# Kernel tuning notes

Measured on AMD Instinct MI355X. Metric: run time of the kernel, lower is better.

Reference implementation:

```python
import jax, jax.numpy as jnp
import numpy as np
from jax import lax

GAMMA = 2.0
BLANK = 0
NEG = -1e30  # log-space 'zero'
T, B, C, L = 1000, 64, 256, 100


def setup_inputs() -> dict:
    key = jax.random.key(0)
    k1, k2 = jax.random.split(key)
    # valid log-probabilities, as produced by a model's log_softmax head
    log_probs = jax.nn.log_softmax(jax.random.normal(k1, (T, B, C), dtype=jnp.float32), axis=-1)
    # concatenated targets, blank (0) excluded as CTC requires
    targets = jax.random.randint(k2, (B * L,), 1, C, dtype=jnp.int32)
    input_lengths = jnp.full((B,), T, dtype=jnp.int32)
    target_lengths = jnp.full((B,), L, dtype=jnp.int32)
    return {"log_probs": log_probs, "targets": targets,
            "input_lengths": input_lengths, "target_lengths": target_lengths}


def _ctc_loss(log_probs, targets2d, input_lengths, target_lengths):
    # log_probs: (T,B,C); targets2d: (B,L). Returns per-sample NLL (B,).
    Tt, Bb, _ = log_probs.shape
    Ll = targets2d.shape[1]
    S = 2 * Ll + 1  # extended label sequence: blank interleaved
    ext = jnp.full((Bb, S), BLANK, dtype=jnp.int32).at[:, 1::2].set(targets2d)
    # emission log-probs for each extended symbol: (T,B,S)
    emit = jnp.take_along_axis(log_probs, jnp.broadcast_to(ext[None], (Tt, Bb, S)), axis=2)
    # skip-transition allowed where symbol is non-blank and differs from s-2
    allow2 = jnp.concatenate(
        [jnp.zeros((Bb, 2), bool), (ext[:, 2:] != BLANK) & (ext[:, 2:] != ext[:, :-2])], axis=1)

    def shiftk(a, k):
        return jnp.pad(a, ((0, 0), (k, 0)), constant_values=NEG)[:, :S]

    alpha0 = jnp.full((Bb, S), NEG, jnp.float32).at[:, 0].set(emit[0, :, 0]).at[:, 1].set(emit[0, :, 1])

    def step(alpha, e):
        a1 = shiftk(alpha, 1)
        a2 = jnp.where(allow2, shiftk(alpha, 2), NEG)
        m = jnp.maximum(jnp.maximum(alpha, a1), a2)
        new = m + jnp.log(jnp.exp(alpha - m) + jnp.exp(a1 - m) + jnp.exp(a2 - m)) + e
        return new, new

    _, rest = lax.scan(step, alpha0, emit[1:])
    alphas = jnp.concatenate([alpha0[None], rest], axis=0)  # (T,B,S)
    b = jnp.arange(Bb)
    last = alphas[input_lengths - 1, b]  # (B,S) at each sample's final step
    ll = jnp.logaddexp(last[b, 2 * target_lengths], last[b, 2 * target_lengths - 1])
    # zero_infinity=True semantics
    return jnp.where(ll > NEG / 2, -ll, 0.0)


def reference(log_probs, targets, input_lengths, target_lengths):
    targets2d = targets.reshape(B, L)
    loss = _ctc_loss(log_probs, targets2d, input_lengths, target_lengths)  # (B,)
    # focal weights: mean-over-time prob of each target symbol (computed under no_grad in torch)
    mean_probs = jnp.exp(log_probs).mean(axis=0)  # (B,C)
    target_probs = lax.stop_gradient(
        jnp.take_along_axis(mean_probs, targets2d, axis=1).reshape(-1))  # (B*L,)
    focal_weight = (1.0 - target_probs) ** GAMMA
    # torch broadcasting quirk: (total,) * (B,1) -> (B,total); mean over all
    return (focal_weight[None, :] * loss[:, None]).mean()
```

## Files before the change

kernel.cpp:

```cpp
#include <hip/hip_runtime.h>
#include <cstdint>

#define T_DIM 1000
#define B_DIM 64
#define C_DIM 256
#define L_DIM 100
#define S_DIM (2 * L_DIM + 1)
#define CH 32
#define NPROD 7
#define RPW 5
#define EMW 132
#define NBLK (2 * B_DIM)

typedef float f32x4 __attribute__((ext_vector_type(4)));

#define DPP_I(x, ctrl) __builtin_amdgcn_update_dpp(0, (x), (ctrl), 0xF, 0xF, true)
#define DPP_F(x, ctrl) __int_as_float(DPP_I(__float_as_int(x), (ctrl)))

#define DSR(dst, addr, OFF) \
    asm volatile("ds_read_b32 %0, %1 offset:" OFF : "=v"(dst) : "v"(addr))
#define ISS(s, OFF) do { DSR(pb##s, apb, OFF); DSR(qa##s, aq1, OFF); DSR(qb##s, aq3, OFF); } while (0)
#define W(N) do { asm volatile("s_waitcnt lgkmcnt(" N ")"); __builtin_amdgcn_sched_barrier(0); } while (0)
#define STP(s) step(pb##s, qa##s, qb##s)
#define SD(s, OFF) do { W("12"); STP(s); ISS(s, OFF); } while (0)

__device__ __forceinline__ float wave_max_dpp(float x) {
    x = fmaxf(x, DPP_F(x, 0x111));
    x = fmaxf(x, DPP_F(x, 0x112));
    x = fmaxf(x, DPP_F(x, 0x114));
    x = fmaxf(x, DPP_F(x, 0x118));
    x = fmaxf(x, DPP_F(x, 0x142));
    x = fmaxf(x, DPP_F(x, 0x143));
    return __int_as_float(__builtin_amdgcn_readlane(__float_as_int(x), 63));
}

__global__ __launch_bounds__(512, 1) void ctc_fused(
        const float* __restrict__ lp,
        const int* __restrict__ tgt,
        const int* __restrict__ il,
        const int* __restrict__ tl,
        float* __restrict__ ws,
        float* __restrict__ out) {
    const int blk = blockIdx.x;
    const int tid = threadIdx.x;
    const uint32_t rstride = B_DIM * C_DIM;

    if (blk >= B_DIM) {
        __shared__ float sums[8][C_DIM];
        __shared__ float meanp[C_DIM];
        __shared__ float focal[128];
        const int b = blk - B_DIM;
        const int lane = tid & 63;
        const int wv = tid >> 6;
        const float* p = lp + (size_t)b * C_DIM + (lane << 2);
        f32x4 s = {0.f, 0.f, 0.f, 0.f};
#pragma unroll 5
        for (int t = wv; t < T_DIM; t += 8) {
            f32x4 v = *(const f32x4*)(p + (size_t)t * rstride);
            s.x += __expf(v.x); s.y += __expf(v.y);
            s.z += __expf(v.z); s.w += __expf(v.w);
        }
        *(f32x4*)&sums[wv][lane << 2] = s;
        __syncthreads();
        if (tid < C_DIM) {
            const float tot = sums[0][tid] + sums[1][tid] + sums[2][tid] + sums[3][tid]
                            + sums[4][tid] + sums[5][tid] + sums[6][tid] + sums[7][tid];
            meanp[tid] = tot * (1.0f / T_DIM);
        }
        __syncthreads();
        if (tid < L_DIM) {
            const float pv = meanp[tgt[b * L_DIM + tid]];
            const float w = 1.0f - pv;
            focal[tid] = w * w;
        }
        __syncthreads();
        if (tid < 64) {
            float fs = focal[tid] + ((tid + 64 < L_DIM) ? focal[tid + 64] : 0.f);
#pragma unroll
            for (int off = 32; off > 0; off >>= 1) fs += __shfl_down(fs, off, 64);
            if (tid == 0) atomicAdd(&ws[0], fs);
        }
    } else {
        __shared__ __align__(16) float emit[2][CH][EMW];

        const int lane = tid & 63;
        const int wave = tid >> 6;
        const int b = blk;
        const int* trow = tgt + b * L_DIM;
        const int ilen = il[b];
        const int tlen = tl[b];

        const int i1 = 2 * lane;
        const int i3 = 2 * lane + 1;
        const int c1 = (i1 < L_DIM) ? trow[i1] : 0;
        const int c3 = (i3 < L_DIM) ? trow[i3] : 0;
        const int c1m = (i1 >= 1 && i1 - 1 < L_DIM) ? trow[i1 - 1] : -1;
        const float m1 = ((i1 >= 1) && (c1 != c1m)) ? 1.0f : 0.0f;
        const float m3 = (c3 != c1) ? 1.0f : 0.0f;

        const float f0 = (4 * lane + 0 < S_DIM) ? 1.0f : 0.0f;
        const float f1 = (4 * lane + 1 < S_DIM) ? 1.0f : 0.0f;
        const float f2 = (4 * lane + 2 < S_DIM) ? 1.0f : 0.0f;
        const float f3 = (4 * lane + 3 < S_DIM) ? 1.0f : 0.0f;

        const float* base = lp + (size_t)b * C_DIM;

        float a0 = 0.f, a1 = 0.f, a2 = 0.f, a3 = 0.f;
        {
            float i0 = __expf(base[0]);
            float i1v = __expf(base[c1]);
            if (lane == 0 && wave == 0) { a0 = i0; a1 = i1v; }
        }
        float ls = 0.f;

        auto produce = [&](int cc) {
            const int p = cc & 1;
            const int tstart = 1 + cc * CH;
            const int w = wave - 1;
            float v1[RPW], v3[RPW], v0[RPW];
#pragma unroll
            for (int k = 0; k < RPW; ++k) {
                const int d = w + NPROD * k;
                if (d < CH) {
                    int t = tstart + d; t = (t < ilen) ? t : (ilen - 1);
                    const float* rp = base + (size_t)t * rstride;
                    v1[k] = rp[c1];
                    v3[k] = rp[c3];
                    v0[k] = rp[0];
                } else {
                    v1[k] = 0.f; v3[k] = 0.f; v0[k] = 0.f;
                }
            }
            asm volatile("" : "+v"(v1[0]), "+v"(v1[1]), "+v"(v1[2]), "+v"(v1[3]), "+v"(v1[4]),
                              "+v"(v3[0]), "+v"(v3[1]), "+v"(v3[2]), "+v"(v3[3]), "+v"(v3[4]),
                              "+v"(v0[0]), "+v"(v0[1]), "+v"(v0[2]), "+v"(v0[3]), "+v"(v0[4]));
#pragma unroll
            for (int k = 0; k < RPW; ++k) {
                const int d = w + NPROD * k;
                if (d < CH) {
                    const float e1 = __expf(v1[k]);
                    const float e3 = __expf(v3[k]);
                    const float e0 = __expf(v0[k]);
                    emit[p][d][lane] = e1;
                    emit[p][d][64 + lane] = e3;
                    if (lane == 0) emit[p][d][128] = e0;
                }
            }
        };

        auto step = [&](float pb, float p1e, float p3e) {
            const float p3 = DPP_F(a3, 0x138);
            const float a01 = a0 + a1;
            const float n0 = (a0 + p3) * pb;
            const float n1 = fmaf(m1, p3, a01) * p1e;
            const float n2 = (a2 + a1) * pb;
            const float n3 = (fmaf(m3, a1, a2) + a3) * p3e;
            a0 = n0; a1 = n1; a2 = n2; a3 = n3;
        };

#define RENORM() do {                                                       \
        a0 *= f0; a1 *= f1; a2 *= f2; a3 *= f3;                             \
        const float mx = wave_max_dpp(fmaxf(fmaxf(a0, a1), fmaxf(a2, a3))); \
        const float inv = __builtin_amdgcn_rcpf(mx);                        \
        ls -= __logf(inv);                                                  \
        a0 *= inv; a1 *= inv; a2 *= inv; a3 *= inv;                         \
    } while (0)

        auto consume = [&](int cc) {
            const int p = cc & 1;
            const int tstart = 1 + cc * CH;
            if (tstart + CH <= ilen) {
                const uint32_t lbase =
                    (uint32_t)(uintptr_t)(&emit[0][0][0]) + (uint32_t)(p * (CH * EMW * 4));
                uint32_t apb = lbase + 512;
                uint32_t aq1 = lbase + ((uint32_t)lane << 2);
                uint32_t aq3 = aq1 + 256;
                float pb0, pb1, pb2, pb3, pb4;
                float qa0, qa1, qa2, qa3, qa4;
                float qb0, qb1, qb2, qb3, qb4;
                ISS(0, "0"); ISS(1, "528"); ISS(2, "1056"); ISS(3, "1584"); ISS(4, "2112");
                SD(0, "2640");
                SD(1, "3168");
                SD(2, "3696");
                SD(3, "4224");
                SD(4, "4752");
                SD(0, "5280");
                SD(1, "5808");
                SD(2, "6336"); RENORM();
                SD(3, "6864");
                SD(4, "7392");
                SD(0, "7920");
                SD(1, "8448");
                SD(2, "8976");
                SD(3, "9504");
                SD(4, "10032");
                SD(0, "10560"); RENORM();
                SD(1, "11088");
                SD(2, "11616");
                SD(3, "12144");
                SD(4, "12672");
                SD(0, "13200");
                SD(1, "13728");
                SD(2, "14256");
                SD(3, "14784"); RENORM();
                SD(4, "15312");
                SD(0, "15840");
                SD(1, "16368");
                W("12"); STP(2);
                W("9");  STP(3);
                W("6");  STP(4);
                W("3");  STP(0);
                W("0");  STP(1); RENORM();
            } else {
#pragma unroll
                for (int d = 0; d < CH; ++d) {
                    if (tstart + d < ilen) {
                        step(emit[p][d][128], emit[p][d][lane], emit[p][d][64 + lane]);
                        if ((d & 7) == 7) RENORM();
                    }
                }
            }
        };

        const int nchunks = (ilen - 1 + CH - 1) / CH;
        if (wave != 0) produce(0);
        __syncthreads();
        if (wave == 0) __builtin_amdgcn_s_setprio(1);
        for (int c = 0; c < nchunks; ++c) {
            if (wave != 0) produce(c + 1);
            else consume(c);
            __syncthreads();
        }
        if (wave == 0) __builtin_amdgcn_s_setprio(0);
#undef RENORM

        if (wave == 0) {
            const int s_hi = 2 * tlen;
            const int s_lo = 2 * tlen - 1;
            const int slot_hi = s_hi & 3, lane_hi = min(s_hi >> 2, 63);
            const int slot_lo = s_lo & 3, lane_lo = min(s_lo >> 2, 63);
            float chv = (slot_hi == 0) ? a0 : (slot_hi == 1) ? a1 : (slot_hi == 2) ? a2 : a3;
            float clv = (slot_lo == 0) ? a0 : (slot_lo == 1) ? a1 : (slot_lo == 2) ? a2 : a3;
            const float vh = __shfl(chv, lane_hi, 64);
            const float vl = __shfl(clv, lane_lo, 64);
            if (lane == 0) {
                const float s = vh + vl;
                const float loss = (s > 0.f) ? -(__logf(s) + ls) : 0.0f;
                atomicAdd(&ws[1], loss);
            }
        }
    }

    if (tid == 0) {
        asm volatile("s_waitcnt vmcnt(0)");
        unsigned int* ctr = (unsigned int*)ws + 2;
        const unsigned int old = atomicAdd(ctr, 1u);
        if (old == NBLK - 1) {
            const float F = atomicAdd(&ws[0], 0.0f);
            const float Lo = atomicAdd(&ws[1], 0.0f);
            out[0] = (F / (float)(B_DIM * L_DIM)) * (Lo / (float)B_DIM);
        }
    }
}

extern "C" void kernel_launch(void* const* d_in, const int* in_sizes, int n_in,
                              void* d_out, int out_size, void* d_ws, size_t ws_size,
                              hipStream_t stream) {
    const float* lp = (const float*)d_in[0];
    const int* tgt = (const int*)d_in[1];
    const int* il = (const int*)d_in[2];
    const int* tl = (const int*)d_in[3];
    float* ws = (float*)d_ws;

    hipMemsetAsync(ws, 0, 3 * sizeof(float), stream);
    ctc_fused<<<dim3(NBLK), dim3(512), 0, stream>>>(
        lp, tgt, il, tl, ws, (float*)d_out);
}
```

Baseline: 135.5 us.

## Replace producer-consumer LDS pipeline with single-wave direct global prefetch ring

Drops the seven producer waves that staged exponentiated emissions through double-buffered shared memory behind block barriers. A single wave now issues its own global loads eight timesteps ahead with inline asm, waits on vmcnt, and runs exp plus the recurrence inline. This removes the __syncthreads and LDS round trips from the serial critical path. In exchange the exp work and global-load latency land on the lone recurrence wave, and the fast path hardcodes ilen == T_DIM and a 65536-byte row stride.

Result: slower. 153.4 us (+13.2%).

```diff
diff --git a/kernel.cpp b/kernel.cpp
--- a/kernel.cpp
+++ b/kernel.cpp
@@ -6,10 +6,6 @@
 #define C_DIM 256
 #define L_DIM 100
 #define S_DIM (2 * L_DIM + 1)
-#define CH 32
-#define NPROD 7
-#define RPW 5
-#define EMW 132
 #define NBLK (2 * B_DIM)
 
 typedef float f32x4 __attribute__((ext_vector_type(4)));
@@ -17,12 +13,20 @@
 #define DPP_I(x, ctrl) __builtin_amdgcn_update_dpp(0, (x), (ctrl), 0xF, 0xF, true)
 #define DPP_F(x, ctrl) __int_as_float(DPP_I(__float_as_int(x), (ctrl)))
 
-#define DSR(dst, addr, OFF) \
-    asm volatile("ds_read_b32 %0, %1 offset:" OFF : "=v"(dst) : "v"(addr))
-#define ISS(s, OFF) do { DSR(pb##s, apb, OFF); DSR(qa##s, aq1, OFF); DSR(qb##s, aq3, OFF); } while (0)
-#define W(N) do { asm volatile("s_waitcnt lgkmcnt(" N ")"); __builtin_amdgcn_sched_barrier(0); } while (0)
-#define STP(s) step(pb##s, qa##s, qb##s)
-#define SD(s, OFF) do { W("12"); STP(s); ISS(s, OFF); } while (0)
+#define GLD(dst, voff) \
+    asm volatile("global_load_dword %0, %1, %2" : "=v"(dst) : "v"(voff), "s"(lp))
+#define WV(N) do { asm volatile("s_waitcnt vmcnt(" N ")"); __builtin_amdgcn_sched_barrier(0); } while (0)
+#define ISSUE(s) do { GLD(g0_##s, o0); GLD(g1_##s, o1); GLD(g3_##s, o3); \
+                      o0 += 65536u; o1 += 65536u; o3 += 65536u; } while (0)
+#define SFULL(s) do { WV("21"); \
+        const float e0 = __expf(g0_##s), e1 = __expf(g1_##s), e3 = __expf(g3_##s); \
+        step(e0, e1, e3); ISSUE(s); } while (0)
+#define SLAST(s) do { WV("21"); \
+        const float e0 = __expf(g0_##s), e1 = __expf(g1_##s), e3 = __expf(g3_##s); \
+        step(e0, e1, e3); } while (0)
+#define STAIL(s, N) do { WV(N); \
+        const float e0 = __expf(g0_##s), e1 = __expf(g1_##s), e3 = __expf(g3_##s); \
+        step(e0, e1, e3); } while (0)
 
 __device__ __forceinline__ float wave_max_dpp(float x) {
     x = fmaxf(x, DPP_F(x, 0x111));
@@ -80,11 +84,8 @@
             for (int off = 32; off > 0; off >>= 1) fs += __shfl_down(fs, off, 64);
             if (tid == 0) atomicAdd(&ws[0], fs);
         }
-    } else {
-        __shared__ __align__(16) float emit[2][CH][EMW];
-
-        const int lane = tid & 63;
-        const int wave = tid >> 6;
+    } else if (tid < 64) {
+        const int lane = tid;
         const int b = blk;
         const int* trow = tgt + b * L_DIM;
         const int ilen = il[b];
@@ -109,44 +110,9 @@
         {
             float i0 = __expf(base[0]);
             float i1v = __expf(base[c1]);
-            if (lane == 0 && wave == 0) { a0 = i0; a1 = i1v; }
+            if (lane == 0) { a0 = i0; a1 = i1v; }
         }
         float ls = 0.f;
-
-        auto produce = [&](int cc) {
-            const int p = cc & 1;
-            const int tstart = 1 + cc * CH;
-            const int w = wave - 1;
-            float v1[RPW], v3[RPW], v0[RPW];
-#pragma unroll
-            for (int k = 0; k < RPW; ++k) {
-                const int d = w + NPROD * k;
-                if (d < CH) {
-                    int t = tstart + d; t = (t < ilen) ? t : (ilen - 1);
-                    const float* rp = base + (size_t)t * rstride;
-                    v1[k] = rp[c1];
-                    v3[k] = rp[c3];
-                    v0[k] = rp[0];
-                } else {
-                    v1[k] = 0.f; v3[k] = 0.f; v0[k] = 0.f;
-                }
-            }
-            asm volatile("" : "+v"(v1[0]), "+v"(v1[1]), "+v"(v1[2]), "+v"(v1[3]), "+v"(v1[4]),
-                              "+v"(v3[0]), "+v"(v3[1]), "+v"(v3[2]), "+v"(v3[3]), "+v"(v3[4]),
-                              "+v"(v0[0]), "+v"(v0[1]), "+v"(v0[2]), "+v"(v0[3]), "+v"(v0[4]));
-#pragma unroll
-            for (int k = 0; k < RPW; ++k) {
-                const int d = w + NPROD * k;
-                if (d < CH) {
-                    const float e1 = __expf(v1[k]);
-                    const float e3 = __expf(v3[k]);
-                    const float e0 = __expf(v0[k]);
-                    emit[p][d][lane] = e1;
-                    emit[p][d][64 + lane] = e3;
-                    if (lane == 0) emit[p][d][128] = e0;
-                }
-            }
-        };
 
         auto step = [&](float pb, float p1e, float p3e) {
             const float p3 = DPP_F(a3, 0x138);
@@ -166,88 +132,47 @@
         a0 *= inv; a1 *= inv; a2 *= inv; a3 *= inv;                         \
     } while (0)
 
-        auto consume = [&](int cc) {
-            const int p = cc & 1;
-            const int tstart = 1 + cc * CH;
-            if (tstart + CH <= ilen) {
-                const uint32_t lbase =
-                    (uint32_t)(uintptr_t)(&emit[0][0][0]) + (uint32_t)(p * (CH * EMW * 4));
-                uint32_t apb = lbase + 512;
-                uint32_t aq1 = lbase + ((uint32_t)lane << 2);
-                uint32_t aq3 = aq1 + 256;
-                float pb0, pb1, pb2, pb3, pb4;
-                float qa0, qa1, qa2, qa3, qa4;
-                float qb0, qb1, qb2, qb3, qb4;
-                ISS(0, "0"); ISS(1, "528"); ISS(2, "1056"); ISS(3, "1584"); ISS(4, "2112");
-                SD(0, "2640");
-                SD(1, "3168");
-                SD(2, "3696");
-                SD(3, "4224");
-                SD(4, "4752");
-                SD(0, "5280");
-                SD(1, "5808");
-                SD(2, "6336"); RENORM();
-                SD(3, "6864");
-                SD(4, "7392");
-                SD(0, "7920");
-                SD(1, "8448");
-                SD(2, "8976");
-                SD(3, "9504");
-                SD(4, "10032");
-                SD(0, "10560"); RENORM();
-                SD(1, "11088");
-                SD(2, "11616");
-                SD(3, "12144");
-                SD(4, "12672");
-                SD(0, "13200");
-                SD(1, "13728");
-                SD(2, "14256");
-                SD(3, "14784"); RENORM();
-                SD(4, "15312");
-                SD(0, "15840");
-                SD(1, "16368");
-                W("12"); STP(2);
-                W("9");  STP(3);
-                W("6");  STP(4);
-                W("3");  STP(0);
-                W("0");  STP(1); RENORM();
-            } else {
-#pragma unroll
-                for (int d = 0; d < CH; ++d) {
-                    if (tstart + d < ilen) {
-                        step(emit[p][d][128], emit[p][d][lane], emit[p][d][64 + lane]);
-                        if ((d & 7) == 7) RENORM();
-                    }
-                }
+        if (ilen == T_DIM) {
+            float g0_0, g0_1, g0_2, g0_3, g0_4, g0_5, g0_6, g0_7;
+            float g1_0, g1_1, g1_2, g1_3, g1_4, g1_5, g1_6, g1_7;
+            float g3_0, g3_1, g3_2, g3_3, g3_4, g3_5, g3_6, g3_7;
+            const uint32_t bc = (uint32_t)b * C_DIM * 4u;
+            uint32_t o0 = bc + 65536u;
+            uint32_t o1 = bc + 65536u + ((uint32_t)c1 << 2);
+            uint32_t o3 = bc + 65536u + ((uint32_t)c3 << 2);
+            ISSUE(0); ISSUE(1); ISSUE(2); ISSUE(3);
+            ISSUE(4); ISSUE(5); ISSUE(6); ISSUE(7);
+            for (int m = 0; m < 123; ++m) {
+                SFULL(0); SFULL(1); SFULL(2); SFULL(3);
+                SFULL(4); SFULL(5); SFULL(6); SFULL(7);
+                RENORM();
             }
-        };
-
-        const int nchunks = (ilen - 1 + CH - 1) / CH;
-        if (wave != 0) produce(0);
-        __syncthreads();
-        if (wave == 0) __builtin_amdgcn_s_setprio(1);
-        for (int c = 0; c < nchunks; ++c) {
-            if (wave != 0) produce(c + 1);
-            else consume(c);
-            __syncthreads();
-        }
-        if (wave == 0) __builtin_amdgcn_s_setprio(0);
+            SFULL(0); SFULL(1); SFULL(2); SFULL(3);
+            SFULL(4); SFULL(5); SFULL(6); SLAST(7);
+            RENORM();
+            STAIL(0, "18"); STAIL(1, "15"); STAIL(2, "12"); STAIL(3, "9");
+            STAIL(4, "6");  STAIL(5, "3");  STAIL(6, "0");
+        } else {
+            for (int t = 1; t < ilen; ++t) {
+                const float* rp = base + (size_t)t * rstride;
+                step(__expf(rp[0]), __expf(rp[c1]), __expf(rp[c3]));
+                if ((t & 7) == 0) RENORM();
+            }
+        }
 #undef RENORM
 
-        if (wave == 0) {
-            const int s_hi = 2 * tlen;
-            const int s_lo = 2 * tlen - 1;
-            const int slot_hi = s_hi & 3, lane_hi = min(s_hi >> 2, 63);
-            const int slot_lo = s_lo & 3, lane_lo = min(s_lo >> 2, 63);
-            float chv = (slot_hi == 0) ? a0 : (slot_hi == 1) ? a1 : (slot_hi == 2) ? a2 : a3;
-            float clv = (slot_lo == 0) ? a0 : (slot_lo == 1) ? a1 : (slot_lo == 2) ? a2 : a3;
-            const float vh = __shfl(chv, lane_hi, 64);
-            const float vl = __shfl(clv, lane_lo, 64);
-            if (lane == 0) {
-                const float s = vh + vl;
-                const float loss = (s > 0.f) ? -(__logf(s) + ls) : 0.0f;
-                atomicAdd(&ws[1], loss);
-            }
+        const int s_hi = 2 * tlen;
+        const int s_lo = 2 * tlen - 1;
+        const int slot_hi = s_hi & 3, lane_hi = min(s_hi >> 2, 63);
+        const int slot_lo = s_lo & 3, lane_lo = min(s_lo >> 2, 63);
+        float chv = (slot_hi == 0) ? a0 : (slot_hi == 1) ? a1 : (slot_hi == 2) ? a2 : a3;
+        float clv = (slot_lo == 0) ? a0 : (slot_lo == 1) ? a1 : (slot_lo == 2) ? a2 : a3;
+        const float vh = __shfl(chv, lane_hi, 64);
+        const float vl = __shfl(clv, lane_lo, 64);
+        if (lane == 0) {
+            const float s = vh + vl;
+            const float loss = (s > 0.f) ? -(__logf(s) + ls) : 0.0f;
+            atomicAdd(&ws[1], loss);
         }
     }
 
```

## Interleave emission tiles for 128-bit LDS reads in CTC consumer loop

Applied to the files above, without the earlier changes.

Changes the shared-memory emission buffer layout so each lane's four consecutive timesteps sit contiguously, and rewrites the consumer's software pipeline to use ds_read_b128 (three wide reads per four steps instead of twelve scalar reads). The aim is to cut LDS instruction count and waitcnt stalls on the serial alpha-recursion critical path of wave 0. In exchange, producer stores become strided 4-byte writes, which may raise bank conflicts on the producer side, and the pipeline is only two groups deep.

New measurement: 133.5 us. Within noise of the previous version (-1.4%).

```diff
diff --git a/kernel.cpp b/kernel.cpp
--- a/kernel.cpp
+++ b/kernel.cpp
@@ -9,7 +9,6 @@
 #define CH 32
 #define NPROD 7
 #define RPW 5
-#define EMW 132
 #define NBLK (2 * B_DIM)
 
 typedef float f32x4 __attribute__((ext_vector_type(4)));
@@ -17,12 +16,13 @@
 #define DPP_I(x, ctrl) __builtin_amdgcn_update_dpp(0, (x), (ctrl), 0xF, 0xF, true)
 #define DPP_F(x, ctrl) __int_as_float(DPP_I(__float_as_int(x), (ctrl)))
 
-#define DSR(dst, addr, OFF) \
-    asm volatile("ds_read_b32 %0, %1 offset:" OFF : "=v"(dst) : "v"(addr))
-#define ISS(s, OFF) do { DSR(pb##s, apb, OFF); DSR(qa##s, aq1, OFF); DSR(qb##s, aq3, OFF); } while (0)
+#define DSR4(dst, addr, OFF) \
+    asm volatile("ds_read_b128 %0, %1 offset:" OFF : "=v"(dst) : "v"(addr))
+#define ISSG(r, QOFF, POFF) do { DSR4(Q1##r, aq1, QOFF); DSR4(Q3##r, aq3, QOFF); \
+                                 DSR4(PB##r, apb, POFF); } while (0)
 #define W(N) do { asm volatile("s_waitcnt lgkmcnt(" N ")"); __builtin_amdgcn_sched_barrier(0); } while (0)
-#define STP(s) step(pb##s, qa##s, qb##s)
-#define SD(s, OFF) do { W("12"); STP(s); ISS(s, OFF); } while (0)
+#define S4(r) do { step(PB##r.x, Q1##r.x, Q3##r.x); step(PB##r.y, Q1##r.y, Q3##r.y); \
+                   step(PB##r.z, Q1##r.z, Q3##r.z); step(PB##r.w, Q1##r.w, Q3##r.w); } while (0)
 
 __device__ __forceinline__ float wave_max_dpp(float x) {
     x = fmaxf(x, DPP_F(x, 0x111));
@@ -81,7 +81,9 @@
             if (tid == 0) atomicAdd(&ws[0], fs);
         }
     } else {
-        __shared__ __align__(16) float emit[2][CH][EMW];
+        __shared__ __align__(16) float q1t[2][8][64][4];
+        __shared__ __align__(16) float q3t[2][8][64][4];
+        __shared__ __align__(16) float pbt[2][8][4];
 
         const int lane = tid & 63;
         const int wave = tid >> 6;
@@ -141,9 +143,9 @@
                     const float e1 = __expf(v1[k]);
                     const float e3 = __expf(v3[k]);
                     const float e0 = __expf(v0[k]);
-                    emit[p][d][lane] = e1;
-                    emit[p][d][64 + lane] = e3;
-                    if (lane == 0) emit[p][d][128] = e0;
+                    q1t[p][d >> 2][lane][d & 3] = e1;
+                    q3t[p][d >> 2][lane][d & 3] = e3;
+                    if (lane == 0) pbt[p][d >> 2][d & 3] = e0;
                 }
             }
         };
@@ -170,52 +172,29 @@
             const int p = cc & 1;
             const int tstart = 1 + cc * CH;
             if (tstart + CH <= ilen) {
-                const uint32_t lbase =
-                    (uint32_t)(uintptr_t)(&emit[0][0][0]) + (uint32_t)(p * (CH * EMW * 4));
-                uint32_t apb = lbase + 512;
-                uint32_t aq1 = lbase + ((uint32_t)lane << 2);
-                uint32_t aq3 = aq1 + 256;
-                float pb0, pb1, pb2, pb3, pb4;
-                float qa0, qa1, qa2, qa3, qa4;
-                float qb0, qb1, qb2, qb3, qb4;
-                ISS(0, "0"); ISS(1, "528"); ISS(2, "1056"); ISS(3, "1584"); ISS(4, "2112");
-                SD(0, "2640");
-                SD(1, "3168");
-                SD(2, "3696");
-                SD(3, "4224");
-                SD(4, "4752");
-                SD(0, "5280");
-                SD(1, "5808");
-                SD(2, "6336"); RENORM();
-                SD(3, "6864");
-                SD(4, "7392");
-                SD(0, "7920");
-                SD(1, "8448");
-                SD(2, "8976");
-                SD(3, "9504");
-                SD(4, "10032");
-                SD(0, "10560"); RENORM();
-                SD(1, "11088");
-                SD(2, "11616");
-                SD(3, "12144");
-                SD(4, "12672");
-                SD(0, "13200");
-                SD(1, "13728");
-                SD(2, "14256");
-                SD(3, "14784"); RENORM();
-                SD(4, "15312");
-                SD(0, "15840");
-                SD(1, "16368");
-                W("12"); STP(2);
-                W("9");  STP(3);
-                W("6");  STP(4);
-                W("3");  STP(0);
-                W("0");  STP(1); RENORM();
+                uint32_t aq1 = (uint32_t)(uintptr_t)(&q1t[0][0][0][0])
+                             + (uint32_t)(p * 8192) + ((uint32_t)lane << 4);
+                uint32_t aq3 = (uint32_t)(uintptr_t)(&q3t[0][0][0][0])
+                             + (uint32_t)(p * 8192) + ((uint32_t)lane << 4);
+                uint32_t apb = (uint32_t)(uintptr_t)(&pbt[0][0][0])
+                             + (uint32_t)(p * 128);
+                f32x4 Q1A, Q3A, PBA, Q1B, Q3B, PBB;
+                ISSG(A, "0", "0"); ISSG(B, "1024", "16");
+                W("3"); S4(A); ISSG(A, "2048", "32");
+                W("3"); S4(B); RENORM(); ISSG(B, "3072", "48");
+                W("3"); S4(A); ISSG(A, "4096", "64");
+                W("3"); S4(B); RENORM(); ISSG(B, "5120", "80");
+                W("3"); S4(A); ISSG(A, "6144", "96");
+                W("3"); S4(B); RENORM(); ISSG(B, "7168", "112");
+                W("3"); S4(A);
+                W("0"); S4(B); RENORM();
             } else {
 #pragma unroll
                 for (int d = 0; d < CH; ++d) {
                     if (tstart + d < ilen) {
-                        step(emit[p][d][128], emit[p][d][lane], emit[p][d][64 + lane]);
+                        step(pbt[p][d >> 2][d & 3],
+                             q1t[p][d >> 2][lane][d & 3],
+                             q3t[p][d >> 2][lane][d & 3]);
                         if ((d & 7) == 7) RENORM();
                     }
                 }
```
